# Optimization experiments

Measured on AMD Instinct MI355X. Metric: run time of the kernel, lower is better.

Reference implementation:

```python
import jax, jax.numpy as jnp
import numpy as np

B, T, C, FREQ = 32, 512, 22, 192
HID = 128


def setup_inputs() -> dict:
    key = jax.random.key(0)
    k1, k2, k3, k4, k5, k6 = jax.random.split(key, 6)
    x = jax.random.normal(k1, (B, T, C, FREQ), dtype=jnp.float32)
    A = jax.random.uniform(k2, (B, T, C, C), dtype=jnp.float32)
    # Linear weights (torch layout: [out, in]); scaled like torch default init
    W0 = jax.random.normal(k3, (HID, FREQ), dtype=jnp.float32) / np.sqrt(FREQ)
    b0 = jax.random.normal(k4, (HID,), dtype=jnp.float32) * 0.01
    W1 = jax.random.normal(k5, (HID, HID), dtype=jnp.float32) / np.sqrt(HID)
    b1 = jax.random.normal(k6, (HID,), dtype=jnp.float32) * 0.01
    return {"x": x, "A": A, "W0": W0, "b0": b0, "W1": W1, "b1": b1}


def reference(x, A, W0, b0, W1, b1):
    # Vectorized over B and T simultaneously (original python-loops over t).
    # Layer i: xt = relu(Linear(bmm(A_t, xt)))
    h = x  # [B,T,C,Freq]
    for W, b in ((W0, b0), (W1, b1)):
        h = jnp.einsum('btij,btjf->btif', A, h)          # adjacency mix over nodes
        h = jax.nn.relu(jnp.einsum('btcf,hf->btch', h, W) + b)  # Linear + ReLU
    # stack over t is implicit; mean over node dim C -> [B,T,HID]
    return h.mean(axis=2)
```

## Files before the change

### kernel.cpp

```cpp
#include <hip/hip_runtime.h>

#define CC 22
#define FF 192
#define HH 128
#define NBT (32 * 512)

typedef __attribute__((ext_vector_type(8))) __bf16 bf16x8;
typedef __attribute__((ext_vector_type(8))) short s16x8;
typedef __attribute__((ext_vector_type(4))) float f32x4;

__device__ __forceinline__ float bf2f(unsigned short u) {
    union { unsigned int i; float f; } v;
    v.i = ((unsigned int)u) << 16;
    return v.f;
}

__device__ __forceinline__ unsigned short f2bf(float f) {
    union { float f; unsigned int i; } v;
    v.f = f;
    return (unsigned short)((v.i + 0x7fffu + ((v.i >> 16) & 1u)) >> 16);
}

__device__ __forceinline__ void split2(float v, unsigned short& h, unsigned short& l) {
    h = f2bf(v);
    float r = v - bf2f(h);
    l = f2bf(r);
}

__device__ __forceinline__ unsigned int cvt_pk_bf16(float a, float b) {
    unsigned int r;
    asm("v_cvt_pk_bf16_f32 %0, %1, %2" : "=v"(r) : "v"(a), "v"(b));
    return r;
}

__device__ __forceinline__ void split_pk2(float a, float b,
                                          unsigned int& hi, unsigned int& lo) {
    hi = cvt_pk_bf16(a, b);
    union { unsigned int i; float f; } ha, hb;
    ha.i = hi << 16;
    hb.i = hi & 0xffff0000u;
    lo = cvt_pk_bf16(a - ha.f, b - hb.f);
}

__device__ __forceinline__ bf16x8 bzero8() {
    s16x8 z = {0, 0, 0, 0, 0, 0, 0, 0};
    return __builtin_bit_cast(bf16x8, z);
}

__device__ __forceinline__ int ybyte(int row, int b) {
    return row * 64 + (b ^ (((row >> 1) & 3) << 4));
}

__device__ __forceinline__ int inputs_are_bf16(const unsigned short* __restrict__ A,
                                               int tid) {
    const float v = bf2f(A[tid & 63]);
    return __all(v >= 0.0f && v <= 1.0001f);
}

// ... 71 lines not shown
            for (int i = 0; i < 11; ++i) {
                const float4 xv = *(const float4*)&sH1[(2 * i + ty) * FF + 4 * fq];
                acc[i] = fmaf(xv.x, u.x, fmaf(xv.y, u.y, fmaf(xv.z, u.z, fmaf(xv.w, u.w, acc[i]))));
            }
        }
        #pragma unroll
        for (int i = 0; i < 11; ++i)
            sH2[(2 * i + ty) * HH + h] = fmaxf(acc[i], 0.f);
    }
    __syncthreads();

    for (int idx4 = tid; idx4 < CC * HH / 4; idx4 += 256) {
        const int c  = idx4 / (HH / 4);
        const int kq = idx4 - c * (HH / 4);
        float4 acc = make_float4(0.f, 0.f, 0.f, 0.f);
        #pragma unroll
        for (int j = 0; j < CC; ++j) {
            const float  a  = sA[c * CC + j];
            const float4 xv = *(const float4*)&sH2[j * HH + 4 * kq];
            acc.x += a * xv.x; acc.y += a * xv.y;
            acc.z += a * xv.z; acc.w += a * xv.w;
        }
        ((float4*)sH3)[idx4] = acc;
    }
    __syncthreads();

    {
        float acc[11];
        const float bb = b1g[h];
        #pragma unroll
        for (int i = 0; i < 11; ++i) acc[i] = bb;
        #pragma unroll 4
        for (int kq = 0; kq < HH / 4; ++kq) {
            float4 u = ((const float4*)(W1g + h * HH))[kq];
            #pragma unroll
            for (int i = 0; i < 11; ++i) {
                const float4 xv = *(const float4*)&sH3[(2 * i + ty) * HH + 4 * kq];
                acc[i] = fmaf(xv.x, u.x, fmaf(xv.y, u.y, fmaf(xv.z, u.z, fmaf(xv.w, u.w, acc[i]))));
            }
        }
        float s = 0.f;
        #pragma unroll
        for (int i = 0; i < 11; ++i) s += fmaxf(acc[i], 0.f);
        sRed[ty * HH + h] = s;
    }
    __syncthreads();

    if (ty == 0) {
        const float m = (sRed[h] + sRed[HH + h]) * (1.0f / 22.0f);
        outg[(size_t)bt * HH + h] = m;
    }
}

__device__ void run_block_split(
    const float* __restrict__ xg, const float* __restrict__ Ag,
    const float* __restrict__ b0g, const float* __restrict__ b1g,
    const unsigned short* __restrict__ wsW,
    float* __restrict__ outg, int bt, int tid, char* smem)
{
    unsigned short* sxh  = (unsigned short*)smem;
    unsigned short* sxl  = (unsigned short*)(smem + 8800);
    unsigned short* sAh  = (unsigned short*)(smem + 17600);
    unsigned short* sAl  = (unsigned short*)(smem + 20160);
    char*           syh  = smem + 22720;
    char*           syl  = smem + 30912;
    unsigned short* sh3h = (unsigned short*)smem;
    unsigned short* sh3l = (unsigned short*)(smem + 8704);

    const unsigned short* W0h = wsW + WS0H;
    const unsigned short* W0l = wsW + WS0L;
    const unsigned short* W1h = wsW + WS1H;
    const unsigned short* W1l = wsW + WS1L;

    {
        const float4* xp4 = (const float4*)(xg + (size_t)bt * (CC * FF));
        for (int idx = tid; idx < CC * (FF / 4); idx += 256) {
            const int c = idx / (FF / 4);
            const int q = idx - c * (FF / 4);
            const float4 v = xp4[idx];
            uint2 hv, lv;
            split_pk2(v.x, v.y, hv.x, lv.x);
            split_pk2(v.z, v.w, hv.y, lv.y);
            *(uint2*)&sxh[c * 200 + 4 * q] = hv;
            *(uint2*)&sxl[c * 200 + 4 * q] = lv;
        }
        const float* Ap = Ag + (size_t)bt * (CC * CC);
        for (int idx = tid; idx < 32 * 40; idx += 256) {
            const int r = idx / 40;
            const int c = idx - r * 40;
            unsigned short h = 0, l = 0;
            if (r < CC && c < CC) split2(Ap[r * CC + c], h, l);
            sAh[idx] = h;
            sAl[idx] = l;
        }
    }
    __syncthreads();

    const int lane = tid & 63;
    const int wid  = tid >> 6;
    const int lr   = lane & 15;
    const int lk   = lane >> 4;
    const int hb   = wid * 32;

    const f32x4 vzero = {0.f, 0.f, 0.f, 0.f};

    {
        f32x4 acc[2][2];
        #pragma unroll
        for (int mt = 0; mt < 2; ++mt)
            #pragma unroll
            for (int nt = 0; nt < 2; ++nt) acc[mt][nt] = vzero;

        #pragma unroll
        for (int ks = 0; ks < 6; ++ks) {
            bf16x8 xfh[2], xfl[2];
            #pragma unroll
            for (int mt = 0; mt < 2; ++mt) {
                const int row = mt * 16 + lr;
                const int rr  = (row < CC) ? row : 0;
                const int off = rr * 200 + ks * 32 + lk * 8;
                bf16x8 fh = *(const bf16x8*)(sxh + off);
                bf16x8 fl = *(const bf16x8*)(sxl + off);
                if (row >= CC) { fh = bzero8(); fl = bzero8(); }
                xfh[mt] = fh; xfl[mt] = fl;
            }
            bf16x8 wfh[2], wfl[2];
            #pragma unroll
            for (int nt = 0; nt < 2; ++nt) {
                const int hcol = hb + nt * 16 + lr;
                const int off  = hcol * FF + ks * 32 + lk * 8;
                wfh[nt] = *(const bf16x8*)(W0h + off);
                wfl[nt] = *(const bf16x8*)(W0l + off);
            }
            #pragma unroll
            for (int mt = 0; mt < 2; ++mt)
                #pragma unroll
                for (int nt = 0; nt < 2; ++nt) {
                    acc[mt][nt] = __builtin_amdgcn_mfma_f32_16x16x32_bf16(xfh[mt], wfh[nt], acc[mt][nt], 0, 0, 0);
                    acc[mt][nt] = __builtin_amdgcn_mfma_f32_16x16x32_bf16(xfl[mt], wfh[nt], acc[mt][nt], 0, 0, 0);
                    acc[mt][nt] = __builtin_amdgcn_mfma_f32_16x16x32_bf16(xfh[mt], wfl[nt], acc[mt][nt], 0, 0, 0);
                }
        }
        #pragma unroll
        for (int mt = 0; mt < 2; ++mt)
            #pragma unroll
            for (int nt = 0; nt < 2; ++nt) {
                const int hcol = hb + nt * 16 + lr;
                uint2 hv, lv;
                split_pk2(acc[mt][nt][0], acc[mt][nt][1], hv.x, lv.x);
                split_pk2(acc[mt][nt][2], acc[mt][nt][3], hv.y, lv.y);
                const int boff = ybyte(hcol, mt * 32 + lk * 8);
                *(uint2*)(syh + boff) = hv;
                *(uint2*)(syl + boff) = lv;
            }
    }
    __syncthreads();

    bf16x8 Afh[2], Afl[2];
    #pragma unroll
    for (int t = 0; t < 2; ++t) {
        const int off = (t * 16 + lr) * 40 + lk * 8;
        Afh[t] = *(const bf16x8*)(sAh + off);
        Afl[t] = *(const bf16x8*)(sAl + off);
    }

    {
        f32x4 acc[2][2];
        #pragma unroll
        for (int nt = 0; nt < 2; ++nt) {
            const float b = b0g[hb + nt * 16 + lr];
            const f32x4 bv = {b, b, b, b};
            acc[0][nt] = bv;
            acc[1][nt] = bv;
        }
        bf16x8 yfh[2], yfl[2];
        #pragma unroll
        for (int nt = 0; nt < 2; ++nt) {
            const int boff = ybyte(hb + nt * 16 + lr, lk * 16);
            yfh[nt] = *(const bf16x8*)(syh + boff);
            yfl[nt] = *(const bf16x8*)(syl + boff);
        }
        asm volatile("" ::: "memory");
        #pragma unroll
        for (int mt = 0; mt < 2; ++mt)
            #pragma unroll
            for (int nt = 0; nt < 2; ++nt) {
                acc[mt][nt] = __builtin_amdgcn_mfma_f32_16x16x32_bf16(Afh[mt], yfh[nt], acc[mt][nt], 0, 0, 0);
                acc[mt][nt] = __builtin_amdgcn_mfma_f32_16x16x32_bf16(Afl[mt], yfh[nt], acc[mt][nt], 0, 0, 0);
                acc[mt][nt] = __builtin_amdgcn_mfma_f32_16x16x32_bf16(Afh[mt], yfl[nt], acc[mt][nt], 0, 0, 0);
            }
        #pragma unroll
        for (int mt = 0; mt < 2; ++mt)
            #pragma unroll
            for (int nt = 0; nt < 2; ++nt) {
                const int hcol = hb + nt * 16 + lr;
                uint2 hv, lv;
                split_pk2(fmaxf(acc[mt][nt][0], 0.f), fmaxf(acc[mt][nt][1], 0.f), hv.x, lv.x);
                split_pk2(fmaxf(acc[mt][nt][2], 0.f), fmaxf(acc[mt][nt][3], 0.f), hv.y, lv.y);
                const int boff = ybyte(hcol, mt * 32 + lk * 8);
                *(uint2*)(syh + boff) = hv;
                *(uint2*)(syl + boff) = lv;
            }
    }

    {
        f32x4 acc[2][2];
        #pragma unroll
        for (int mt = 0; mt < 2; ++mt)
            #pragma unroll
            for (int ct = 0; ct < 2; ++ct) acc[mt][ct] = vzero;

        bf16x8 gfh[2], gfl[2];
        #pragma unroll
        for (int mt = 0; mt < 2; ++mt) {
            const int boff = ybyte(hb + mt * 16 + lr, lk * 16);
            gfh[mt] = *(const bf16x8*)(syh + boff);
            gfl[mt] = *(const bf16x8*)(syl + boff);
        }
        #pragma unroll
        for (int mt = 0; mt < 2; ++mt)
            #pragma unroll
            for (int ct = 0; ct < 2; ++ct) {
                acc[mt][ct] = __builtin_amdgcn_mfma_f32_16x16x32_bf16(gfh[mt], Afh[ct], acc[mt][ct], 0, 0, 0);
                acc[mt][ct] = __builtin_amdgcn_mfma_f32_16x16x32_bf16(gfl[mt], Afh[ct], acc[mt][ct], 0, 0, 0);
                acc[mt][ct] = __builtin_amdgcn_mfma_f32_16x16x32_bf16(gfh[mt], Afl[ct], acc[mt][ct], 0, 0, 0);
            }
        #pragma unroll
        for (int mt = 0; mt < 2; ++mt)
            #pragma unroll
            for (int ct = 0; ct < 2; ++ct) {
                const int cp = ct * 16 + lr;
                uint2 hv, lv;
                split_pk2(acc[mt][ct][0], acc[mt][ct][1], hv.x, lv.x);
                split_pk2(acc[mt][ct][2], acc[mt][ct][3], hv.y, lv.y);
                const int e = cp * 136 + hb + mt * 16 + lk * 4;
                *(uint2*)&sh3h[e] = hv;
                *(uint2*)&sh3l[e] = lv;
            }
    }
    __syncthreads();

    {
        f32x4 acc[2][2];
        #pragma unroll
        for (int mt = 0; mt < 2; ++mt) {
            const float4 bv = *(const float4*)(b1g + hb + mt * 16 + lk * 4);
            const f32x4 bb = {bv.x, bv.y, bv.z, bv.w};
            acc[mt][0] = bb;
            acc[mt][1] = bb;
        }
        #pragma unroll
        for (int ks = 0; ks < 4; ++ks) {
            bf16x8 wfh[2], wfl[2], hfh[2], hfl[2];
            #pragma unroll
            for (int mt = 0; mt < 2; ++mt) {
                const int o   = hb + mt * 16 + lr;
                const int off = o * HH + ks * 32 + lk * 8;
                wfh[mt] = *(const bf16x8*)(W1h + off);
                wfl[mt] = *(const bf16x8*)(W1l + off);
            }
            #pragma unroll
            for (int ct = 0; ct < 2; ++ct) {
                const int off = (ct * 16 + lr) * 136 + ks * 32 + lk * 8;
                hfh[ct] = *(const bf16x8*)(sh3h + off);
                hfl[ct] = *(const bf16x8*)(sh3l + off);
            }
            #pragma unroll
            for (int mt = 0; mt < 2; ++mt)
                #pragma unroll
                for (int ct = 0; ct < 2; ++ct) {
                    acc[mt][ct] = __builtin_amdgcn_mfma_f32_16x16x32_bf16(wfh[mt], hfh[ct], acc[mt][ct], 0, 0, 0);
                    acc[mt][ct] = __builtin_amdgcn_mfma_f32_16x16x32_bf16(wfl[mt], hfh[ct], acc[mt][ct], 0, 0, 0);
                    acc[mt][ct] = __builtin_amdgcn_mfma_f32_16x16x32_bf16(wfh[mt], hfl[ct], acc[mt][ct], 0, 0, 0);
                }
        }
        float s[2][4];
        #pragma unroll
        for (int mt = 0; mt < 2; ++mt)
            #pragma unroll
            for (int r = 0; r < 4; ++r) {
                float v = fmaxf(acc[mt][0][r], 0.f);
                if (lr < CC - 16) v += fmaxf(acc[mt][1][r], 0.f);
                s[mt][r] = v;
            }
        #pragma unroll
        for (int m = 1; m < 16; m <<= 1)
            #pragma unroll
            for (int mt = 0; mt < 2; ++mt)
                #pragma unroll
                for (int r = 0; r < 4; ++r)
                    s[mt][r] += __shfl_xor(s[mt][r], m);

        if (lr == 0) {
            const float inv = 1.0f / 22.0f;
            #pragma unroll
            for (int mt = 0; mt < 2; ++mt) {
                float4 o4;
                o4.x = s[mt][0] * inv;
                o4.y = s[mt][1] * inv;
                o4.z = s[mt][2] * inv;
                o4.w = s[mt][3] * inv;
                *(float4*)(outg + (size_t)bt * HH + hb + mt * 16 + lk * 4) = o4;
            }
        }
    }
}

__device__ void run_block_bf16(
    const unsigned short* __restrict__ xg, const unsigned short* __restrict__ Ag,
    const unsigned short* __restrict__ W0g, const unsigned short* __restrict__ b0g,
    const unsigned short* __restrict__ W1g, const unsigned short* __restrict__ b1g,
    unsigned short* __restrict__ outg, int bt, int tid, char* smem)
{
    unsigned short* sXT  = (unsigned short*)smem;
    unsigned short* sAm  = (unsigned short*)(smem + 15360);
    unsigned short* sH1  = (unsigned short*)(smem + 17920);
    unsigned short* sH2T = (unsigned short*)smem;
    unsigned short* sH3  = (unsigned short*)(smem + 17920);

    const unsigned short* xp = xg + (size_t)bt * (CC * FF);
    const unsigned short* Ap = Ag + (size_t)bt * (CC * CC);

    for (int id = tid; id < 32 * 40; id += 256) {
        const int r = id / 40;
        const int c = id - r * 40;
        sAm[id] = (r < CC && c < CC) ? Ap[r * CC + c] : (unsigned short)0;
    }
    for (int id = tid; id < FF * 9; id += 256) {
        const int f = id / 9;
        const int q = id - f * 9;
        ((unsigned int*)sXT)[f * 20 + 11 + q] = 0u;
    }
    for (int id = tid; id < 24 * CC; id += 256) {
        const int fb = id / CC;
        const int j  = id - fb * CC;
        const uint4 v = *(const uint4*)(xp + j * FF + fb * 8);
        unsigned short* d = sXT + (fb * 8) * 40 + j;
        d[0 * 40] = (unsigned short)(v.x & 0xffffu);
        d[1 * 40] = (unsigned short)(v.x >> 16);
        d[2 * 40] = (unsigned short)(v.y & 0xffffu);
        d[3 * 40] = (unsigned short)(v.y >> 16);
        d[4 * 40] = (unsigned short)(v.z & 0xffffu);
        d[5 * 40] = (unsigned short)(v.z >> 16);
        d[6 * 40] = (unsigned short)(v.w & 0xffffu);
        d[7 * 40] = (unsigned short)(v.w >> 16);
    }
    __syncthreads();

    const int lane = tid & 63;
    const int wid  = tid >> 6;
    const int lr   = lane & 15;
    const int lk   = lane >> 4;
    const f32x4 vzero = {0.f, 0.f, 0.f, 0.f};

    {
        f32x4 acc[3][2];
        #pragma unroll
        for (int i = 0; i < 3; ++i)
            #pragma unroll
            for (int j = 0; j < 2; ++j) acc[i][j] = vzero;
        bf16x8 xa[3], ab[2];
        #pragma unroll
        for (int i = 0; i < 3; ++i)
            xa[i] = *(const bf16x8*)(sXT + ((3 * wid + i) * 16 + lr) * 40 + lk * 8);
        #pragma unroll
        for (int j = 0; j < 2; ++j)
            ab[j] = *(const bf16x8*)(sAm + (j * 16 + lr) * 40 + lk * 8);
        #pragma unroll
        for (int i = 0; i < 3; ++i)
            #pragma unroll
            for (int j = 0; j < 2; ++j)
                acc[i][j] = __builtin_amdgcn_mfma_f32_16x16x32_bf16(xa[i], ab[j], acc[i][j], 0, 0, 0);
        #pragma unroll
        for (int i = 0; i < 3; ++i) {
            const int fbase = (3 * wid + i) * 16 + lk * 4;
            #pragma unroll
            for (int j = 0; j < 2; ++j) {
                const int c = j * 16 + lr;
                ushort4 st;
                st.x = f2bf(acc[i][j][0]);
                st.y = f2bf(acc[i][j][1]);
                st.z = f2bf(acc[i][j][2]);
                st.w = f2bf(acc[i][j][3]);
                *(ushort4*)(sH1 + c * 200 + fbase) = st;
            }
        }
    }
    __syncthreads();

    {
        f32x4 acc[2][2];
        #pragma unroll
        for (int nt = 0; nt < 2; ++nt) {
            const float bv = bf2f(b0g[(2 * wid + nt) * 16 + lr]);
            f32x4 bvv = {bv, bv, bv, bv};
            acc[0][nt] = bvv;
            acc[1][nt] = bvv;
        }
        #pragma unroll
        for (int ks = 0; ks < 6; ++ks) {
            bf16x8 af[2], bfr[2];
            #pragma unroll
            for (int mt = 0; mt < 2; ++mt)
                af[mt] = *(const bf16x8*)(sH1 + (mt * 16 + lr) * 200 + ks * 32 + lk * 8);
            #pragma unroll
            for (int nt = 0; nt < 2; ++nt)
                bfr[nt] = *(const bf16x8*)(W0g + ((size_t)((2 * wid + nt) * 16 + lr)) * FF + ks * 32 + lk * 8);
            #pragma unroll
            for (int mt = 0; mt < 2; ++mt)
                #pragma unroll
                for (int nt = 0; nt < 2; ++nt)
                    acc[mt][nt] = __builtin_amdgcn_mfma_f32_16x16x32_bf16(af[mt], bfr[nt], acc[mt][nt], 0, 0, 0);
        }
        #pragma unroll
        for (int mt = 0; mt < 2; ++mt) {
            const int cbase = mt * 16 + lk * 4;
            #pragma unroll
            for (int nt = 0; nt < 2; ++nt) {
                const int hcol = (2 * wid + nt) * 16 + lr;
                ushort4 st;
                st.x = (cbase + 0 < CC) ? f2bf(fmaxf(acc[mt][nt][0], 0.f)) : (unsigned short)0;
                st.y = (cbase + 1 < CC) ? f2bf(fmaxf(acc[mt][nt][1], 0.f)) : (unsigned short)0;
                st.z = (cbase + 2 < CC) ? f2bf(fmaxf(acc[mt][nt][2], 0.f)) : (unsigned short)0;
                st.w = (cbase + 3 < CC) ? f2bf(fmaxf(acc[mt][nt][3], 0.f)) : (unsigned short)0;
                *(ushort4*)(sH2T + hcol * 40 + cbase) = st;
            }
        }
    }
    __syncthreads();

    {
        f32x4 acc[2][2];
        #pragma unroll
        for (int mt = 0; mt < 2; ++mt)
            #pragma unroll
            for (int ct = 0; ct < 2; ++ct) acc[mt][ct] = vzero;
        bf16x8 af[2], bb[2];
        #pragma unroll
        for (int mt = 0; mt < 2; ++mt)
            af[mt] = *(const bf16x8*)(sH2T + ((2 * wid + mt) * 16 + lr) * 40 + lk * 8);
        #pragma unroll
        for (int ct = 0; ct < 2; ++ct)
            bb[ct] = *(const bf16x8*)(sAm + (ct * 16 + lr) * 40 + lk * 8);
        #pragma unroll
        for (int mt = 0; mt < 2; ++mt)
            #pragma unroll
            for (int ct = 0; ct < 2; ++ct)
                acc[mt][ct] = __builtin_amdgcn_mfma_f32_16x16x32_bf16(af[mt], bb[ct], acc[mt][ct], 0, 0, 0);
        __syncthreads();
        #pragma unroll
        for (int mt = 0; mt < 2; ++mt) {
            const int hbase = (2 * wid + mt) * 16 + lk * 4;
            #pragma unroll
            for (int ct = 0; ct < 2; ++ct) {
                const int c = ct * 16 + lr;
                ushort4 st;
                st.x = f2bf(acc[mt][ct][0]);
                st.y = f2bf(acc[mt][ct][1]);
                st.z = f2bf(acc[mt][ct][2]);
                st.w = f2bf(acc[mt][ct][3]);
                *(ushort4*)(sH3 + c * 136 + hbase) = st;
            }
        }
    }
    __syncthreads();

    {
        f32x4 acc[2][2];
        #pragma unroll
        for (int mt = 0; mt < 2; ++mt) {
            const ushort4 bu = *(const ushort4*)(b1g + (2 * wid + mt) * 16 + lk * 4);
            f32x4 bvv = {bf2f(bu.x), bf2f(bu.y), bf2f(bu.z), bf2f(bu.w)};
            acc[mt][0] = bvv;
            acc[mt][1] = bvv;
        }
        #pragma unroll
        for (int ks = 0; ks < 4; ++ks) {
            bf16x8 af[2], bfr[2];
            #pragma unroll
            for (int mt = 0; mt < 2; ++mt)
                af[mt] = *(const bf16x8*)(W1g + ((size_t)((2 * wid + mt) * 16 + lr)) * HH + ks * 32 + lk * 8);
            #pragma unroll
            for (int ct = 0; ct < 2; ++ct)
                bfr[ct] = *(const bf16x8*)(sH3 + (ct * 16 + lr) * 136 + ks * 32 + lk * 8);
            #pragma unroll
            for (int mt = 0; mt < 2; ++mt)
                #pragma unroll
                for (int ct = 0; ct < 2; ++ct)
                    acc[mt][ct] = __builtin_amdgcn_mfma_f32_16x16x32_bf16(af[mt], bfr[ct], acc[mt][ct], 0, 0, 0);
        }
        float s[2][4];
        #pragma unroll
        for (int mt = 0; mt < 2; ++mt)
            #pragma unroll
            for (int r = 0; r < 4; ++r) {
                float v = fmaxf(acc[mt][0][r], 0.f);
                if (lr < CC - 16) v += fmaxf(acc[mt][1][r], 0.f);
                s[mt][r] = v;
            }
        #pragma unroll
        for (int m = 1; m < 16; m <<= 1)
            #pragma unroll
            for (int mt = 0; mt < 2; ++mt)
                #pragma unroll
                for (int r = 0; r < 4; ++r)
                    s[mt][r] += __shfl_xor(s[mt][r], m);
        if (lr == 0) {
            const float inv = 1.0f / 22.0f;
            #pragma unroll
            for (int mt = 0; mt < 2; ++mt) {
                ushort4 st;
                st.x = f2bf(s[mt][0] * inv);
                st.y = f2bf(s[mt][1] * inv);
                st.z = f2bf(s[mt][2] * inv);
                st.w = f2bf(s[mt][3] * inv);
                *(ushort4*)(outg + (size_t)bt * HH + (2 * wid + mt) * 16 + lk * 4) = st;
            }
        }
    }
}

__global__ __launch_bounds__(256) void tgcn_kernel(
    const void* __restrict__ x, const void* __restrict__ A,
    const void* __restrict__ W0, const void* __restrict__ b0,
    const void* __restrict__ W1, const void* __restrict__ b1,
    void* __restrict__ out, const unsigned short* __restrict__ wsW,
    int use_split)
{
    __shared__ __align__(16) char smem[39104];

    const int tid = threadIdx.x;
    const int bt  = blockIdx.x;
    const int isbf = inputs_are_bf16((const unsigned short*)A, tid);

    if (isbf) {
        run_block_bf16((const unsigned short*)x, (const unsigned short*)A,
                       (const unsigned short*)W0, (const unsigned short*)b0,
                       (const unsigned short*)W1, (const unsigned short*)b1,
                       (unsigned short*)out, bt, tid, smem);
    } else if (use_split) {
        run_block_split((const float*)x, (const float*)A,
                        (const float*)b0, (const float*)b1,
                        wsW, (float*)out, bt, tid, smem);
    } else {
        float* sA  = (float*)smem;
        float* sX  = (float*)(smem + 1936);
        float* sH1 = (float*)(smem + 18832);
        run_block_f32((const float*)x, (const float*)A,
                      (const float*)W0, (const float*)b0,
                      (const float*)W1, (const float*)b1,
                      (float*)out, bt, tid, sA, sX, sH1);
    }
}

extern "C" void kernel_launch(void* const* d_in, const int* in_sizes, int n_in,
                              void* d_out, int out_size, void* d_ws, size_t ws_size,
                              hipStream_t stream) {
    unsigned short* wsW = (unsigned short*)d_ws;
    const int use_split = (ws_size >= (size_t)(81920 * 2)) ? 1 : 0;

    if (use_split)
        convert_weights<<<160, 256, 0, stream>>>(
            (const float*)d_in[2], (const float*)d_in[4],
            (const unsigned short*)d_in[1], wsW);
    tgcn_kernel<<<NBT, 256, 0, stream>>>(
        d_in[0], d_in[1], d_in[2], d_in[3], d_in[4], d_in[5], d_out,
        wsW, use_split);
}
```

Before: 701.7 us.

## Make blocks persistent and prefetch next tile's inputs into registers

```diff
diff --git a/kernel.cpp b/kernel.cpp
--- a/kernel.cpp
+++ b/kernel.cpp
@@ -4,6 +4,8 @@
 #define FF 192
 #define HH 128
 #define NBT (32 * 512)
+#define NBLK 2048
+#define NITER (NBT / NBLK)
 
 typedef __attribute__((ext_vector_type(8))) __bf16 bf16x8;
 typedef __attribute__((ext_vector_type(8))) short s16x8;
@@ -181,11 +183,11 @@
     }
 }
 
-__device__ void run_block_split(
+__device__ void run_split_loop(
     const float* __restrict__ xg, const float* __restrict__ Ag,
     const float* __restrict__ b0g, const float* __restrict__ b1g,
     const unsigned short* __restrict__ wsW,
-    float* __restrict__ outg, int bt, int tid, char* smem)
+    float* __restrict__ outg, int blk, int tid, char* smem)
 {
     unsigned short* sxh  = (unsigned short*)smem;
     unsigned short* sxl  = (unsigned short*)(smem + 8800);
@@ -201,29 +203,11 @@
     const unsigned short* W1h = wsW + WS1H;
     const unsigned short* W1l = wsW + WS1L;
 
-    {
-        const float4* xp4 = (const float4*)(xg + (size_t)bt * (CC * FF));
-        for (int idx = tid; idx < CC * (FF / 4); idx += 256) {
-            const int c = idx / (FF / 4);
-            const int q = idx - c * (FF / 4);
-            const float4 v = xp4[idx];
-            uint2 hv, lv;
-            split_pk2(v.x, v.y, hv.x, lv.x);
-            split_pk2(v.z, v.w, hv.y, lv.y);
-            *(uint2*)&sxh[c * 200 + 4 * q] = hv;
-            *(uint2*)&sxl[c * 200 + 4 * q] = lv;
-        }
-        const float* Ap = Ag + (size_t)bt * (CC * CC);
-        for (int idx = tid; idx < 32 * 40; idx += 256) {
-            const int r = idx / 40;
-            const int c = idx - r * 40;
-            unsigned short h = 0, l = 0;
-            if (r < CC && c < CC) split2(Ap[r * CC + c], h, l);
-            sAh[idx] = h;
-            sAl[idx] = l;
-        }
-    }
-    __syncthreads();
+    for (int idx = tid; idx < 32 * 40; idx += 256) {
+        const int r = idx / 40;
+        const int c = idx - r * 40;
+        if (!(r < CC && c < CC)) { sAh[idx] = 0; sAl[idx] = 0; }
+    }
 
     const int lane = tid & 63;
     const int wid  = tid >> 6;
@@ -233,205 +217,277 @@
 
     const f32x4 vzero = {0.f, 0.f, 0.f, 0.f};
 
+    float4 xr0, xr1, xr2, xr3, xr4v;
+    float  a0v, a1v = 0.f;
     {
-        f32x4 acc[2][2];
-        #pragma unroll
-        for (int mt = 0; mt < 2; ++mt)
-            #pragma unroll
-            for (int nt = 0; nt < 2; ++nt) acc[mt][nt] = vzero;
-
-        #pragma unroll
-        for (int ks = 0; ks < 6; ++ks) {
-            bf16x8 xfh[2], xfl[2];
+        const float4* xp4 = (const float4*)xg + (size_t)blk * (CC * FF / 4);
+        xr0 = xp4[tid];
+        xr1 = xp4[tid + 256];
+        xr2 = xp4[tid + 512];
+        xr3 = xp4[tid + 768];
+        if (tid < 32) xr4v = xp4[tid + 1024];
+        const float* Ap = Ag + (size_t)blk * (CC * CC);
+        a0v = Ap[tid];
+        if (tid < CC * CC - 256) a1v = Ap[tid + 256];
+    }
+
+    for (int it = 0; it < NITER; ++it) {
+        const int bt = it * NBLK + blk;
+
+        {
+            float4 xv[4] = {xr0, xr1, xr2, xr3};
+            #pragma unroll
+            for (int k = 0; k < 4; ++k) {
+                const int idx4 = tid + 256 * k;
+                const int c = idx4 / (FF / 4);
+                const int q = idx4 - c * (FF / 4);
+                uint2 hv, lv;
+                split_pk2(xv[k].x, xv[k].y, hv.x, lv.x);
+                split_pk2(xv[k].z, xv[k].w, hv.y, lv.y);
+                *(uint2*)&sxh[c * 200 + 4 * q] = hv;
+                *(uint2*)&sxl[c * 200 + 4 * q] = lv;
+            }
+            if (tid < 32) {
+                const int idx4 = tid + 1024;
+                const int c = idx4 / (FF / 4);
+                const int q = idx4 - c * (FF / 4);
+                uint2 hv, lv;
+                split_pk2(xr4v.x, xr4v.y, hv.x, lv.x);
+                split_pk2(xr4v.z, xr4v.w, hv.y, lv.y);
+                *(uint2*)&sxh[c * 200 + 4 * q] = hv;
+                *(uint2*)&sxl[c * 200 + 4 * q] = lv;
+            }
+            {
+                const int r = tid / CC, c = tid - r * CC;
+                unsigned short h, l;
+                split2(a0v, h, l);
+                sAh[r * 40 + c] = h;
+                sAl[r * 40 + c] = l;
+                if (tid < CC * CC - 256) {
+                    const int i2 = tid + 256;
+                    const int r2 = i2 / CC, c2 = i2 - r2 * CC;
+                    split2(a1v, h, l);
+                    sAh[r2 * 40 + c2] = h;
+                    sAl[r2 * 40 + c2] = l;
+                }
+            }
+        }
+        __syncthreads();
+
+        if (it + 1 < NITER) {
+            const int btn = (it + 1) * NBLK + blk;
+            const float4* xp4 = (const float4*)xg + (size_t)btn * (CC * FF / 4);
+            xr0 = xp4[tid];
+            xr1 = xp4[tid + 256];
+            xr2 = xp4[tid + 512];
+            xr3 = xp4[tid + 768];
+            if (tid < 32) xr4v = xp4[tid + 1024];
+            const float* Ap = Ag + (size_t)btn * (CC * CC);
+            a0v = Ap[tid];
+            if (tid < CC * CC - 256) a1v = Ap[tid + 256];
+        }
+
+        bf16x8 Afh[2], Afl[2];
+        #pragma unroll
+        for (int t = 0; t < 2; ++t) {
+            const int off = (t * 16 + lr) * 40 + lk * 8;
+            Afh[t] = *(const bf16x8*)(sAh + off);
+            Afl[t] = *(const bf16x8*)(sAl + off);
+        }
+
+        {
+            f32x4 acc[2][2];
+            #pragma unroll
+            for (int mt = 0; mt < 2; ++mt)
+                #pragma unroll
+                for (int nt = 0; nt < 2; ++nt) acc[mt][nt] = vzero;
+
+            #pragma unroll
+            for (int ks = 0; ks < 6; ++ks) {
+                bf16x8 xfh[2], xfl[2];
+                #pragma unroll
+                for (int mt = 0; mt < 2; ++mt) {
+                    const int row = mt * 16 + lr;
+                    const int rr  = (row < CC) ? row : 0;
+                    const int off = rr * 200 + ks * 32 + lk * 8;
+                    bf16x8 fh = *(const bf16x8*)(sxh + off);
+                    bf16x8 fl = *(const bf16x8*)(sxl + off);
+                    if (row >= CC) { fh = bzero8(); fl = bzero8(); }
+                    xfh[mt] = fh; xfl[mt] = fl;
+                }
+                bf16x8 wfh[2], wfl[2];
+                #pragma unroll
+                for (int nt = 0; nt < 2; ++nt) {
+                    const int hcol = hb + nt * 16 + lr;
+                    const int off  = hcol * FF + ks * 32 + lk * 8;
+                    wfh[nt] = *(const bf16x8*)(W0h + off);
+                    wfl[nt] = *(const bf16x8*)(W0l + off);
+                }
+                #pragma unroll
+                for (int mt = 0; mt < 2; ++mt)
+                    #pragma unroll
+                    for (int nt = 0; nt < 2; ++nt) {
+                        acc[mt][nt] = __builtin_amdgcn_mfma_f32_16x16x32_bf16(xfh[mt], wfh[nt], acc[mt][nt], 0, 0, 0);
+                        acc[mt][nt] = __builtin_amdgcn_mfma_f32_16x16x32_bf16(xfl[mt], wfh[nt], acc[mt][nt], 0, 0, 0);
+                        acc[mt][nt] = __builtin_amdgcn_mfma_f32_16x16x32_bf16(xfh[mt], wfl[nt], acc[mt][nt], 0, 0, 0);
+                    }
+            }
+            #pragma unroll
+            for (int mt = 0; mt < 2; ++mt)
+                #pragma unroll
+                for (int nt = 0; nt < 2; ++nt) {
+                    const int hcol = hb + nt * 16 + lr;
+                    uint2 hv, lv;
+                    split_pk2(acc[mt][nt][0], acc[mt][nt][1], hv.x, lv.x);
+                    split_pk2(acc[mt][nt][2], acc[mt][nt][3], hv.y, lv.y);
+                    const int boff = ybyte(hcol, mt * 32 + lk * 8);
+                    *(uint2*)(syh + boff) = hv;
+                    *(uint2*)(syl + boff) = lv;
+                }
+        }
+        __syncthreads();
+
+        {
+            f32x4 acc[2][2];
+            #pragma unroll
+            for (int nt = 0; nt < 2; ++nt) {
+                const float b = b0g[hb + nt * 16 + lr];
+                const f32x4 bv = {b, b, b, b};
+                acc[0][nt] = bv;
+                acc[1][nt] = bv;
+            }
+            bf16x8 yfh[2], yfl[2];
+            #pragma unroll
+            for (int nt = 0; nt < 2; ++nt) {
+                const int boff = ybyte(hb + nt * 16 + lr, lk * 16);
+                yfh[nt] = *(const bf16x8*)(syh + boff);
+                yfl[nt] = *(const bf16x8*)(syl + boff);
+            }
+            asm volatile("" ::: "memory");
+            #pragma unroll
+            for (int mt = 0; mt < 2; ++mt)
+                #pragma unroll
+                for (int nt = 0; nt < 2; ++nt) {
+                    acc[mt][nt] = __builtin_amdgcn_mfma_f32_16x16x32_bf16(Afh[mt], yfh[nt], acc[mt][nt], 0, 0, 0);
+                    acc[mt][nt] = __builtin_amdgcn_mfma_f32_16x16x32_bf16(Afl[mt], yfh[nt], acc[mt][nt], 0, 0, 0);
+                    acc[mt][nt] = __builtin_amdgcn_mfma_f32_16x16x32_bf16(Afh[mt], yfl[nt], acc[mt][nt], 0, 0, 0);
+                }
+            #pragma unroll
+            for (int mt = 0; mt < 2; ++mt)
+                #pragma unroll
+                for (int nt = 0; nt < 2; ++nt) {
+                    const int hcol = hb + nt * 16 + lr;
+                    uint2 hv, lv;
+                    split_pk2(fmaxf(acc[mt][nt][0], 0.f), fmaxf(acc[mt][nt][1], 0.f), hv.x, lv.x);
+                    split_pk2(fmaxf(acc[mt][nt][2], 0.f), fmaxf(acc[mt][nt][3], 0.f), hv.y, lv.y);
+                    const int boff = ybyte(hcol, mt * 32 + lk * 8);
+                    *(uint2*)(syh + boff) = hv;
+                    *(uint2*)(syl + boff) = lv;
+                }
+        }
+
+        {
+            f32x4 acc[2][2];
+            #pragma unroll
+            for (int mt = 0; mt < 2; ++mt)
+                #pragma unroll
+                for (int ct = 0; ct < 2; ++ct) acc[mt][ct] = vzero;
+
+            bf16x8 gfh[2], gfl[2];
             #pragma unroll
             for (int mt = 0; mt < 2; ++mt) {
-                const int row = mt * 16 + lr;
-                const int rr  = (row < CC) ? row : 0;
-                const int off = rr * 200 + ks * 32 + lk * 8;
-                bf16x8 fh = *(const bf16x8*)(sxh + off);
-                bf16x8 fl = *(const bf16x8*)(sxl + off);
-                if (row >= CC) { fh = bzero8(); fl = bzero8(); }
-                xfh[mt] = fh; xfl[mt] = fl;
-            }
-            bf16x8 wfh[2], wfl[2];
-            #pragma unroll
-            for (int nt = 0; nt < 2; ++nt) {
-                const int hcol = hb + nt * 16 + lr;
-                const int off  = hcol * FF + ks * 32 + lk * 8;
-                wfh[nt] = *(const bf16x8*)(W0h + off);
-                wfl[nt] = *(const bf16x8*)(W0l + off);
-            }
-            #pragma unroll
-            for (int mt = 0; mt < 2; ++mt)
-                #pragma unroll
-                for (int nt = 0; nt < 2; ++nt) {
-                    acc[mt][nt] = __builtin_amdgcn_mfma_f32_16x16x32_bf16(xfh[mt], wfh[nt], acc[mt][nt], 0, 0, 0);
-                    acc[mt][nt] = __builtin_amdgcn_mfma_f32_16x16x32_bf16(xfl[mt], wfh[nt], acc[mt][nt], 0, 0, 0);
-                    acc[mt][nt] = __builtin_amdgcn_mfma_f32_16x16x32_bf16(xfh[mt], wfl[nt], acc[mt][nt], 0, 0, 0);
-                }
-        }
-        #pragma unroll
-        for (int mt = 0; mt < 2; ++mt)
-            #pragma unroll
-            for (int nt = 0; nt < 2; ++nt) {
-                const int hcol = hb + nt * 16 + lr;
-                uint2 hv, lv;
-                split_pk2(acc[mt][nt][0], acc[mt][nt][1], hv.x, lv.x);
-                split_pk2(acc[mt][nt][2], acc[mt][nt][3], hv.y, lv.y);
-                const int boff = ybyte(hcol, mt * 32 + lk * 8);
-                *(uint2*)(syh + boff) = hv;
-                *(uint2*)(syl + boff) = lv;
-            }
-    }
-    __syncthreads();
-
-    bf16x8 Afh[2], Afl[2];
-    #pragma unroll
-    for (int t = 0; t < 2; ++t) {
-        const int off = (t * 16 + lr) * 40 + lk * 8;
-        Afh[t] = *(const bf16x8*)(sAh + off);
-        Afl[t] = *(const bf16x8*)(sAl + off);
-    }
-
-    {
-        f32x4 acc[2][2];
-        #pragma unroll
-        for (int nt = 0; nt < 2; ++nt) {
-            const float b = b0g[hb + nt * 16 + lr];
-            const f32x4 bv = {b, b, b, b};
-            acc[0][nt] = bv;
-            acc[1][nt] = bv;
-        }
-        bf16x8 yfh[2], yfl[2];
-        #pragma unroll
-        for (int nt = 0; nt < 2; ++nt) {
-            const int boff = ybyte(hb + nt * 16 + lr, lk * 16);
-            yfh[nt] = *(const bf16x8*)(syh + boff);
-            yfl[nt] = *(const bf16x8*)(syl + boff);
-        }
-        asm volatile("" ::: "memory");
-        #pragma unroll
-        for (int mt = 0; mt < 2; ++mt)
-            #pragma unroll
-            for (int nt = 0; nt < 2; ++nt) {
-                acc[mt][nt] = __builtin_amdgcn_mfma_f32_16x16x32_bf16(Afh[mt], yfh[nt], acc[mt][nt], 0, 0, 0);
-                acc[mt][nt] = __builtin_amdgcn_mfma_f32_16x16x32_bf16(Afl[mt], yfh[nt], acc[mt][nt], 0, 0, 0);
-                acc[mt][nt] = __builtin_amdgcn_mfma_f32_16x16x32_bf16(Afh[mt], yfl[nt], acc[mt][nt], 0, 0, 0);
-            }
-        #pragma unroll
-        for (int mt = 0; mt < 2; ++mt)
-            #pragma unroll
-            for (int nt = 0; nt < 2; ++nt) {
-                const int hcol = hb + nt * 16 + lr;
-                uint2 hv, lv;
-                split_pk2(fmaxf(acc[mt][nt][0], 0.f), fmaxf(acc[mt][nt][1], 0.f), hv.x, lv.x);
-                split_pk2(fmaxf(acc[mt][nt][2], 0.f), fmaxf(acc[mt][nt][3], 0.f), hv.y, lv.y);
-                const int boff = ybyte(hcol, mt * 32 + lk * 8);
-                *(uint2*)(syh + boff) = hv;
-                *(uint2*)(syl + boff) = lv;
-            }
-    }
-
-    {
-        f32x4 acc[2][2];
-        #pragma unroll
-        for (int mt = 0; mt < 2; ++mt)
-            #pragma unroll
-            for (int ct = 0; ct < 2; ++ct) acc[mt][ct] = vzero;
-
-        bf16x8 gfh[2], gfl[2];
-        #pragma unroll
-        for (int mt = 0; mt < 2; ++mt) {
-            const int boff = ybyte(hb + mt * 16 + lr, lk * 16);
-            gfh[mt] = *(const bf16x8*)(syh + boff);
-            gfl[mt] = *(const bf16x8*)(syl + boff);
-        }
-        #pragma unroll
-        for (int mt = 0; mt < 2; ++mt)
-            #pragma unroll
-            for (int ct = 0; ct < 2; ++ct) {
-                acc[mt][ct] = __builtin_amdgcn_mfma_f32_16x16x32_bf16(gfh[mt], Afh[ct], acc[mt][ct], 0, 0, 0);
-                acc[mt][ct] = __builtin_amdgcn_mfma_f32_16x16x32_bf16(gfl[mt], Afh[ct], acc[mt][ct], 0, 0, 0);
-                acc[mt][ct] = __builtin_amdgcn_mfma_f32_16x16x32_bf16(gfh[mt], Afl[ct], acc[mt][ct], 0, 0, 0);
-            }
-        #pragma unroll
-        for (int mt = 0; mt < 2; ++mt)
-            #pragma unroll
-            for (int ct = 0; ct < 2; ++ct) {
-                const int cp = ct * 16 + lr;
-                uint2 hv, lv;
-                split_pk2(acc[mt][ct][0], acc[mt][ct][1], hv.x, lv.x);
-                split_pk2(acc[mt][ct][2], acc[mt][ct][3], hv.y, lv.y);
-                const int e = cp * 136 + hb + mt * 16 + lk * 4;
-                *(uint2*)&sh3h[e] = hv;
-                *(uint2*)&sh3l[e] = lv;
-            }
-    }
-    __syncthreads();
-
-    {
-        f32x4 acc[2][2];
-        #pragma unroll
-        for (int mt = 0; mt < 2; ++mt) {
-            const float4 bv = *(const float4*)(b1g + hb + mt * 16 + lk * 4);
-            const f32x4 bb = {bv.x, bv.y, bv.z, bv.w};
-            acc[mt][0] = bb;
-            acc[mt][1] = bb;
-        }
-        #pragma unroll
-        for (int ks = 0; ks < 4; ++ks) {
-            bf16x8 wfh[2], wfl[2], hfh[2], hfl[2];
+                const int boff = ybyte(hb + mt * 16 + lr, lk * 16);
+                gfh[mt] = *(const bf16x8*)(syh + boff);
+                gfl[mt] = *(const bf16x8*)(syl + boff);
+            }
+            #pragma unroll
+            for (int mt = 0; mt < 2; ++mt)
+                #pragma unroll
+                for (int ct = 0; ct < 2; ++ct) {
+                    acc[mt][ct] = __builtin_amdgcn_mfma_f32_16x16x32_bf16(gfh[mt], Afh[ct], acc[mt][ct], 0, 0, 0);
+                    acc[mt][ct] = __builtin_amdgcn_mfma_f32_16x16x32_bf16(gfl[mt], Afh[ct], acc[mt][ct], 0, 0, 0);
+                    acc[mt][ct] = __builtin_amdgcn_mfma_f32_16x16x32_bf16(gfh[mt], Afl[ct], acc[mt][ct], 0, 0, 0);
+                }
+            #pragma unroll
+            for (int mt = 0; mt < 2; ++mt)
+                #pragma unroll
+                for (int ct = 0; ct < 2; ++ct) {
+                    const int cp = ct * 16 + lr;
+                    uint2 hv, lv;
+                    split_pk2(acc[mt][ct][0], acc[mt][ct][1], hv.x, lv.x);
+                    split_pk2(acc[mt][ct][2], acc[mt][ct][3], hv.y, lv.y);
+                    const int e = cp * 136 + hb + mt * 16 + lk * 4;
+                    *(uint2*)&sh3h[e] = hv;
+                    *(uint2*)&sh3l[e] = lv;
+                }
+        }
+        __syncthreads();
+
+        {
+            f32x4 acc[2][2];
             #pragma unroll
             for (int mt = 0; mt < 2; ++mt) {
-                const int o   = hb + mt * 16 + lr;
-                const int off = o * HH + ks * 32 + lk * 8;
-                wfh[mt] = *(const bf16x8*)(W1h + off);
-                wfl[mt] = *(const bf16x8*)(W1l + off);
-            }
-            #pragma unroll
-            for (int ct = 0; ct < 2; ++ct) {
-                const int off = (ct * 16 + lr) * 136 + ks * 32 + lk * 8;
-                hfh[ct] = *(const bf16x8*)(sh3h + off);
-                hfl[ct] = *(const bf16x8*)(sh3l + off);
-            }
-            #pragma unroll
-            for (int mt = 0; mt < 2; ++mt)
+                const float4 bv = *(const float4*)(b1g + hb + mt * 16 + lk * 4);
+                const f32x4 bb = {bv.x, bv.y, bv.z, bv.w};
+                acc[mt][0] = bb;
+                acc[mt][1] = bb;
+            }
+            #pragma unroll
+            for (int ks = 0; ks < 4; ++ks) {
+                bf16x8 wfh[2], wfl[2], hfh[2], hfl[2];
+                #pragma unroll
+                for (int mt = 0; mt < 2; ++mt) {
+                    const int o   = hb + mt * 16 + lr;
+                    const int off = o * HH + ks * 32 + lk * 8;
+                    wfh[mt] = *(const bf16x8*)(W1h + off);
+                    wfl[mt] = *(const bf16x8*)(W1l + off);
+                }
                 #pragma unroll
                 for (int ct = 0; ct < 2; ++ct) {
-                    acc[mt][ct] = __builtin_amdgcn_mfma_f32_16x16x32_bf16(wfh[mt], hfh[ct], acc[mt][ct], 0, 0, 0);
-                    acc[mt][ct] = __builtin_amdgcn_mfma_f32_16x16x32_bf16(wfl[mt], hfh[ct], acc[mt][ct], 0, 0, 0);
-                    acc[mt][ct] = __builtin_amdgcn_mfma_f32_16x16x32_bf16(wfh[mt], hfl[ct], acc[mt][ct], 0, 0, 0);
-                }
-        }
-        float s[2][4];
-        #pragma unroll
-        for (int mt = 0; mt < 2; ++mt)
-            #pragma unroll
-            for (int r = 0; r < 4; ++r) {
-                float v = fmaxf(acc[mt][0][r], 0.f);
-                if (lr < CC - 16) v += fmaxf(acc[mt][1][r], 0.f);
-                s[mt][r] = v;
-            }
-        #pragma unroll
-        for (int m = 1; m < 16; m <<= 1)
-            #pragma unroll
-            for (int mt = 0; mt < 2; ++mt)
-                #pragma unroll
-                for (int r = 0; r < 4; ++r)
-                    s[mt][r] += __shfl_xor(s[mt][r], m);
-
-        if (lr == 0) {
-            const float inv = 1.0f / 22.0f;
-            #pragma unroll
-            for (int mt = 0; mt < 2; ++mt) {
-                float4 o4;
-                o4.x = s[mt][0] * inv;
-                o4.y = s[mt][1] * inv;
-                o4.z = s[mt][2] * inv;
-                o4.w = s[mt][3] * inv;
-                *(float4*)(outg + (size_t)bt * HH + hb + mt * 16 + lk * 4) = o4;
-            }
-        }
+                    const int off = (ct * 16 + lr) * 136 + ks * 32 + lk * 8;
+                    hfh[ct] = *(const bf16x8*)(sh3h + off);
+                    hfl[ct] = *(const bf16x8*)(sh3l + off);
+                }
+                #pragma unroll
+                for (int mt = 0; mt < 2; ++mt)
+                    #pragma unroll
+                    for (int ct = 0; ct < 2; ++ct) {
+                        acc[mt][ct] = __builtin_amdgcn_mfma_f32_16x16x32_bf16(wfh[mt], hfh[ct], acc[mt][ct], 0, 0, 0);
+                        acc[mt][ct] = __builtin_amdgcn_mfma_f32_16x16x32_bf16(wfl[mt], hfh[ct], acc[mt][ct], 0, 0, 0);
+                        acc[mt][ct] = __builtin_amdgcn_mfma_f32_16x16x32_bf16(wfh[mt], hfl[ct], acc[mt][ct], 0, 0, 0);
+                    }
+            }
+            float s[2][4];
+            #pragma unroll
+            for (int mt = 0; mt < 2; ++mt)
+                #pragma unroll
+                for (int r = 0; r < 4; ++r) {
+                    float v = fmaxf(acc[mt][0][r], 0.f);
+                    if (lr < CC - 16) v += fmaxf(acc[mt][1][r], 0.f);
+                    s[mt][r] = v;
+                }
+            #pragma unroll
+            for (int m = 1; m < 16; m <<= 1)
+                #pragma unroll
+                for (int mt = 0; mt < 2; ++mt)
+                    #pragma unroll
+                    for (int r = 0; r < 4; ++r)
+                        s[mt][r] += __shfl_xor(s[mt][r], m);
+
+            if (lr == 0) {
+                const float inv = 1.0f / 22.0f;
+                #pragma unroll
+                for (int mt = 0; mt < 2; ++mt) {
+                    float4 o4;
+                    o4.x = s[mt][0] * inv;
+                    o4.y = s[mt][1] * inv;
+                    o4.z = s[mt][2] * inv;
+                    o4.w = s[mt][3] * inv;
+                    *(float4*)(outg + (size_t)bt * HH + hb + mt * 16 + lk * 4) = o4;
+                }
+            }
+        }
+        __syncthreads();
     }
 }
 
@@ -441,38 +497,17 @@
     const unsigned short* __restrict__ W1g, const unsigned short* __restrict__ b1g,
     unsigned short* __restrict__ outg, int bt, int tid, char* smem)
 {
-    unsigned short* sXT  = (unsigned short*)smem;
-    unsigned short* sAm  = (unsigned short*)(smem + 15360);
-    unsigned short* sH1  = (unsigned short*)(smem + 17920);
-    unsigned short* sH2T = (unsigned short*)smem;
-    unsigned short* sH3  = (unsigned short*)(smem + 17920);
-
-    const unsigned short* xp = xg + (size_t)bt * (CC * FF);
-    const unsigned short* Ap = Ag + (size_t)bt * (CC * CC);
-
-    for (int id = tid; id < 32 * 40; id += 256) {
-        const int r = id / 40;
-        const int c = id - r * 40;
-        sAm[id] = (r < CC && c < CC) ? Ap[r * CC + c] : (unsigned short)0;
-    }
-    for (int id = tid; id < FF * 9; id += 256) {
-        const int f = id / 9;
-        const int q = id - f * 9;
-        ((unsigned int*)sXT)[f * 20 + 11 + q] = 0u;
-    }
-    for (int id = tid; id < 24 * CC; id += 256) {
-        const int fb = id / CC;
-        const int j  = id - fb * CC;
-        const uint4 v = *(const uint4*)(xp + j * FF + fb * 8);
-        unsigned short* d = sXT + (fb * 8) * 40 + j;
-        d[0 * 40] = (unsigned short)(v.x & 0xffffu);
-        d[1 * 40] = (unsigned short)(v.x >> 16);
-        d[2 * 40] = (unsigned short)(v.y & 0xffffu);
-        d[3 * 40] = (unsigned short)(v.y >> 16);
-        d[4 * 40] = (unsigned short)(v.z & 0xffffu);
-        d[5 * 40] = (unsigned short)(v.z >> 16);
-        d[6 * 40] = (unsigned short)(v.w & 0xffffu);
-        d[7 * 40] = (unsigned short)(v.w >> 16);
+    unsigned short* sAm = (unsigned short*)smem;
+    char*           sy  = smem + 2560;
+    unsigned short* sh3 = (unsigned short*)smem;
+
+    {
+        const unsigned short* Ap = Ag + (size_t)bt * (CC * CC);
+        for (int idx = tid; idx < 32 * 40; idx += 256) {
+            const int r = idx / 40;
+            const int c = idx - r * 40;
+            sAm[idx] = (r < CC && c < CC) ? Ap[r * CC + c] : (unsigned short)0;
+        }
     }
     __syncthreads();
 
@@ -480,83 +515,83 @@
     const int wid  = tid >> 6;
     const int lr   = lane & 15;
     const int lk   = lane >> 4;
+    const int hb   = wid * 32;
     const f32x4 vzero = {0.f, 0.f, 0.f, 0.f};
 
+    bf16x8 Af[2];
+    #pragma unroll
+    for (int t = 0; t < 2; ++t)
+        Af[t] = *(const bf16x8*)(sAm + (t * 16 + lr) * 40 + lk * 8);
+
     {
-        f32x4 acc[3][2];
-        #pragma unroll
-        for (int i = 0; i < 3; ++i)
-            #pragma unroll
-            for (int j = 0; j < 2; ++j) acc[i][j] = vzero;
-        bf16x8 xa[3], ab[2];
-        #pragma unroll
-        for (int i = 0; i < 3; ++i)
-            xa[i] = *(const bf16x8*)(sXT + ((3 * wid + i) * 16 + lr) * 40 + lk * 8);
-        #pragma unroll
-        for (int j = 0; j < 2; ++j)
-            ab[j] = *(const bf16x8*)(sAm + (j * 16 + lr) * 40 + lk * 8);
-        #pragma unroll
-        for (int i = 0; i < 3; ++i)
-            #pragma unroll
-            for (int j = 0; j < 2; ++j)
-                acc[i][j] = __builtin_amdgcn_mfma_f32_16x16x32_bf16(xa[i], ab[j], acc[i][j], 0, 0, 0);
-        #pragma unroll
-        for (int i = 0; i < 3; ++i) {
-            const int fbase = (3 * wid + i) * 16 + lk * 4;
-            #pragma unroll
-            for (int j = 0; j < 2; ++j) {
-                const int c = j * 16 + lr;
-                ushort4 st;
-                st.x = f2bf(acc[i][j][0]);
-                st.y = f2bf(acc[i][j][1]);
-                st.z = f2bf(acc[i][j][2]);
-                st.w = f2bf(acc[i][j][3]);
-                *(ushort4*)(sH1 + c * 200 + fbase) = st;
-            }
-        }
-    }
-    __syncthreads();
+        const unsigned short* xb = xg + (size_t)bt * (CC * FF);
+        f32x4 acc[2][2];
+        #pragma unroll
+        for (int mt = 0; mt < 2; ++mt)
+            #pragma unroll
+            for (int nt = 0; nt < 2; ++nt) acc[mt][nt] = vzero;
+        #pragma unroll
+        for (int ks = 0; ks < 6; ++ks) {
+            bf16x8 xf[2], wf[2];
+            #pragma unroll
+            for (int mt = 0; mt < 2; ++mt) {
+                const int row = mt * 16 + lr;
+                const int rr  = (row < CC) ? row : 0;
+                bf16x8 f = *(const bf16x8*)(xb + rr * FF + ks * 32 + lk * 8);
+                if (row >= CC) f = bzero8();
+                xf[mt] = f;
+            }
+            #pragma unroll
+            for (int nt = 0; nt < 2; ++nt)
+                wf[nt] = *(const bf16x8*)(W0g + ((size_t)(hb + nt * 16 + lr)) * FF + ks * 32 + lk * 8);
+            #pragma unroll
+            for (int mt = 0; mt < 2; ++mt)
+                #pragma unroll
+                for (int nt = 0; nt < 2; ++nt)
+                    acc[mt][nt] = __builtin_amdgcn_mfma_f32_16x16x32_bf16(xf[mt], wf[nt], acc[mt][nt], 0, 0, 0);
+        }
+        #pragma unroll
+        for (int mt = 0; mt < 2; ++mt)
+            #pragma unroll
+            for (int nt = 0; nt < 2; ++nt) {
+                const int hcol = hb + nt * 16 + lr;
+                uint2 hv;
+                hv.x = cvt_pk_bf16(acc[mt][nt][0], acc[mt][nt][1]);
+                hv.y = cvt_pk_bf16(acc[mt][nt][2], acc[mt][nt][3]);
+                *(uint2*)(sy + ybyte(hcol, mt * 32 + lk * 8)) = hv;
+            }
+    }
 
     {
         f32x4 acc[2][2];
         #pragma unroll
         for (int nt = 0; nt < 2; ++nt) {
-            const float bv = bf2f(b0g[(2 * wid + nt) * 16 + lr]);
-            f32x4 bvv = {bv, bv, bv, bv};
-            acc[0][nt] = bvv;
-            acc[1][nt] = bvv;
-        }
-        #pragma unroll
-        for (int ks = 0; ks < 6; ++ks) {
-            bf16x8 af[2], bfr[2];
-            #pragma unroll
-            for (int mt = 0; mt < 2; ++mt)
-                af[mt] = *(const bf16x8*)(sH1 + (mt * 16 + lr) * 200 + ks * 32 + lk * 8);
+            const float b = bf2f(b0g[hb + nt * 16 + lr]);
+            const f32x4 bv = {b, b, b, b};
+            acc[0][nt] = bv;
+            acc[1][nt] = bv;
+        }
+        bf16x8 yf[2];
+        #pragma unroll
+        for (int nt = 0; nt < 2; ++nt)
+            yf[nt] = *(const bf16x8*)(sy + ybyte(hb + nt * 16 + lr, lk * 16));
+        asm volatile("" ::: "memory");
+        #pragma unroll
+        for (int mt = 0; mt < 2; ++mt)
             #pragma unroll
             for (int nt = 0; nt < 2; ++nt)
-                bfr[nt] = *(const bf16x8*)(W0g + ((size_t)((2 * wid + nt) * 16 + lr)) * FF + ks * 32 + lk * 8);
-            #pragma unroll
-            for (int mt = 0; mt < 2; ++mt)
-                #pragma unroll
-                for (int nt = 0; nt < 2; ++nt)
-                    acc[mt][nt] = __builtin_amdgcn_mfma_f32_16x16x32_bf16(af[mt], bfr[nt], acc[mt][nt], 0, 0, 0);
-        }
-        #pragma unroll
-        for (int mt = 0; mt < 2; ++mt) {
-            const int cbase = mt * 16 + lk * 4;
+                acc[mt][nt] = __builtin_amdgcn_mfma_f32_16x16x32_bf16(Af[mt], yf[nt], acc[mt][nt], 0, 0, 0);
+        #pragma unroll
+        for (int mt = 0; mt < 2; ++mt)
             #pragma unroll
             for (int nt = 0; nt < 2; ++nt) {
-                const int hcol = (2 * wid + nt) * 16 + lr;
-                ushort4 st;
-                st.x = (cbase + 0 < CC) ? f2bf(fmaxf(acc[mt][nt][0], 0.f)) : (unsigned short)0;
-                st.y = (cbase + 1 < CC) ? f2bf(fmaxf(acc[mt][nt][1], 0.f)) : (unsigned short)0;
-                st.z = (cbase + 2 < CC) ? f2bf(fmaxf(acc[mt][nt][2], 0.f)) : (unsigned short)0;
-                st.w = (cbase + 3 < CC) ? f2bf(fmaxf(acc[mt][nt][3], 0.f)) : (unsigned short)0;
-                *(ushort4*)(sH2T + hcol * 40 + cbase) = st;
-            }
-        }
-    }
-    __syncthreads();
+                const int hcol = hb + nt * 16 + lr;
+                uint2 hv;
+                hv.x = cvt_pk_bf16(fmaxf(acc[mt][nt][0], 0.f), fmaxf(acc[mt][nt][1], 0.f));
+                hv.y = cvt_pk_bf16(fmaxf(acc[mt][nt][2], 0.f), fmaxf(acc[mt][nt][3], 0.f));
+                *(uint2*)(sy + ybyte(hcol, mt * 32 + lk * 8)) = hv;
+            }
+    }
 
     {
         f32x4 acc[2][2];
@@ -564,33 +599,26 @@
         for (int mt = 0; mt < 2; ++mt)
             #pragma unroll
             for (int ct = 0; ct < 2; ++ct) acc[mt][ct] = vzero;
-        bf16x8 af[2], bb[2];
-        #pragma unroll
-        for (int mt = 0; mt < 2; ++mt)
-            af[mt] = *(const bf16x8*)(sH2T + ((2 * wid + mt) * 16 + lr) * 40 + lk * 8);
-        #pragma unroll
-        for (int ct = 0; ct < 2; ++ct)
-            bb[ct] = *(const bf16x8*)(sAm + (ct * 16 + lr) * 40 + lk * 8);
+        bf16x8 gf[2];
+        #pragma unroll
+        for (int mt = 0; mt < 2; ++mt)
+            gf[mt] = *(const bf16x8*)(sy + ybyte(hb + mt * 16 + lr, lk * 16));
         #pragma unroll
         for (int mt = 0; mt < 2; ++mt)
             #pragma unroll
             for (int ct = 0; ct < 2; ++ct)
-                acc[mt][ct] = __builtin_amdgcn_mfma_f32_16x16x32_bf16(af[mt], bb[ct], acc[mt][ct], 0, 0, 0);
+                acc[mt][ct] = __builtin_amdgcn_mfma_f32_16x16x32_bf16(gf[mt], Af[ct], acc[mt][ct], 0, 0, 0);
         __syncthreads();
         #pragma unroll
-        for (int mt = 0; mt < 2; ++mt) {
-            const int hbase = (2 * wid + mt) * 16 + lk * 4;
+        for (int mt = 0; mt < 2; ++mt)
             #pragma unroll
             for (int ct = 0; ct < 2; ++ct) {
-                const int c = ct * 16 + lr;
-                ushort4 st;
-                st.x = f2bf(acc[mt][ct][0]);
-                st.y = f2bf(acc[mt][ct][1]);
-                st.z = f2bf(acc[mt][ct][2]);
-                st.w = f2bf(acc[mt][ct][3]);
-                *(ushort4*)(sH3 + c * 136 + hbase) = st;
-            }
-        }
+                const int cp = ct * 16 + lr;
+                uint2 hv;
+                hv.x = cvt_pk_bf16(acc[mt][ct][0], acc[mt][ct][1]);
+                hv.y = cvt_pk_bf16(acc[mt][ct][2], acc[mt][ct][3]);
+                *(uint2*)&sh3[cp * 136 + hb + mt * 16 + lk * 4] = hv;
+            }
     }
     __syncthreads();
 
@@ -598,25 +626,25 @@
         f32x4 acc[2][2];
         #pragma unroll
         for (int mt = 0; mt < 2; ++mt) {
-            const ushort4 bu = *(const ushort4*)(b1g + (2 * wid + mt) * 16 + lk * 4);
+            const ushort4 bu = *(const ushort4*)(b1g + hb + mt * 16 + lk * 4);
             f32x4 bvv = {bf2f(bu.x), bf2f(bu.y), bf2f(bu.z), bf2f(bu.w)};
             acc[mt][0] = bvv;
             acc[mt][1] = bvv;
         }
         #pragma unroll
         for (int ks = 0; ks < 4; ++ks) {
-            bf16x8 af[2], bfr[2];
-            #pragma unroll
-            for (int mt = 0; mt < 2; ++mt)
-                af[mt] = *(const bf16x8*)(W1g + ((size_t)((2 * wid + mt) * 16 + lr)) * HH + ks * 32 + lk * 8);
+            bf16x8 wf[2], hf[2];
+            #pragma unroll
+            for (int mt = 0; mt < 2; ++mt)
+                wf[mt] = *(const bf16x8*)(W1g + ((size_t)(hb + mt * 16 + lr)) * HH + ks * 32 + lk * 8);
             #pragma unroll
             for (int ct = 0; ct < 2; ++ct)
-                bfr[ct] = *(const bf16x8*)(sH3 + (ct * 16 + lr) * 136 + ks * 32 + lk * 8);
+                hf[ct] = *(const bf16x8*)(sh3 + (ct * 16 + lr) * 136 + ks * 32 + lk * 8);
             #pragma unroll
             for (int mt = 0; mt < 2; ++mt)
                 #pragma unroll
                 for (int ct = 0; ct < 2; ++ct)
-                    acc[mt][ct] = __builtin_amdgcn_mfma_f32_16x16x32_bf16(af[mt], bfr[ct], acc[mt][ct], 0, 0, 0);
+                    acc[mt][ct] = __builtin_amdgcn_mfma_f32_16x16x32_bf16(wf[mt], hf[ct], acc[mt][ct], 0, 0, 0);
         }
         float s[2][4];
         #pragma unroll
@@ -638,18 +666,16 @@
             const float inv = 1.0f / 22.0f;
             #pragma unroll
             for (int mt = 0; mt < 2; ++mt) {
-                ushort4 st;
-                st.x = f2bf(s[mt][0] * inv);
-                st.y = f2bf(s[mt][1] * inv);
-                st.z = f2bf(s[mt][2] * inv);
-                st.w = f2bf(s[mt][3] * inv);
-                *(ushort4*)(outg + (size_t)bt * HH + (2 * wid + mt) * 16 + lk * 4) = st;
-            }
-        }
-    }
-}
-
-__global__ __launch_bounds__(256) void tgcn_kernel(
+                uint2 st;
+                st.x = cvt_pk_bf16(s[mt][0] * inv, s[mt][1] * inv);
+                st.y = cvt_pk_bf16(s[mt][2] * inv, s[mt][3] * inv);
+                *(uint2*)(outg + (size_t)bt * HH + hb + mt * 16 + lk * 4) = st;
+            }
+        }
+    }
+}
+
+__global__ __launch_bounds__(256, 4) void tgcn_kernel(
     const void* __restrict__ x, const void* __restrict__ A,
     const void* __restrict__ W0, const void* __restrict__ b0,
     const void* __restrict__ W1, const void* __restrict__ b1,
@@ -659,26 +685,32 @@
     __shared__ __align__(16) char smem[39104];
 
     const int tid = threadIdx.x;
-    const int bt  = blockIdx.x;
+    const int blk = blockIdx.x;
     const int isbf = inputs_are_bf16((const unsigned short*)A, tid);
 
     if (isbf) {
-        run_block_bf16((const unsigned short*)x, (const unsigned short*)A,
-                       (const unsigned short*)W0, (const unsigned short*)b0,
-                       (const unsigned short*)W1, (const unsigned short*)b1,
-                       (unsigned short*)out, bt, tid, smem);
+        for (int it = 0; it < NITER; ++it) {
+            run_block_bf16((const unsigned short*)x, (const unsigned short*)A,
+                           (const unsigned short*)W0, (const unsigned short*)b0,
+                           (const unsigned short*)W1, (const unsigned short*)b1,
+                           (unsigned short*)out, it * NBLK + blk, tid, smem);
+            __syncthreads();
+        }
     } else if (use_split) {
-        run_block_split((const float*)x, (const float*)A,
-                        (const float*)b0, (const float*)b1,
-                        wsW, (float*)out, bt, tid, smem);
+        run_split_loop((const float*)x, (const float*)A,
+                       (const float*)b0, (const float*)b1,
+                       wsW, (float*)out, blk, tid, smem);
     } else {
         float* sA  = (float*)smem;
         float* sX  = (float*)(smem + 1936);
         float* sH1 = (float*)(smem + 18832);
-        run_block_f32((const float*)x, (const float*)A,
-                      (const float*)W0, (const float*)b0,
-                      (const float*)W1, (const float*)b1,
-                      (float*)out, bt, tid, sA, sX, sH1);
+        for (int it = 0; it < NITER; ++it) {
+            run_block_f32((const float*)x, (const float*)A,
+                          (const float*)W0, (const float*)b0,
+                          (const float*)W1, (const float*)b1,
+                          (float*)out, it * NBLK + blk, tid, sA, sX, sH1);
+            __syncthreads();
+        }
     }
 }
 
@@ -692,7 +724,7 @@
         convert_weights<<<160, 256, 0, stream>>>(
             (const float*)d_in[2], (const float*)d_in[4],
             (const unsigned short*)d_in[1], wsW);
-    tgcn_kernel<<<NBT, 256, 0, stream>>>(
+    tgcn_kernel<<<NBLK, 256, 0, stream>>>(
         d_in[0], d_in[1], d_in[2], d_in[3], d_in[4], d_in[5], d_out,
         wsW, use_split);
 }
```

After: 708.1 us. About the same (+0.9%).
